# Kernel optimization log

Hardware: AMD Instinct MI355X
Metric: run time of the kernel (lower is better)

## Reference

```python
import jax, jax.numpy as jnp
import numpy as np

B, T, C, H, D = 131072, 8, 32, 4, 8  # batch, context_window, n_embed, num_heads, head_size


def setup_inputs() -> dict:
    key = jax.random.key(0)
    ks = jax.random.split(key, 7)
    s = 0.02
    return {
        "x": jax.random.normal(ks[0], (B, T, C), dtype=jnp.float32),
        "Wq": jax.random.normal(ks[1], (H, C, D), dtype=jnp.float32) * s,
        "Wk": jax.random.normal(ks[2], (H, C, D), dtype=jnp.float32) * s,
        "Wv": jax.random.normal(ks[3], (H, C, D), dtype=jnp.float32) * s,
        "Wf": jax.random.normal(ks[4], (C, C), dtype=jnp.float32) * s,
        "bf": jax.random.normal(ks[5], (C,), dtype=jnp.float32) * s,
    }


def reference(x, Wq, Wk, Wv, Wf, bf):
    # Multi-head causal self-attention (heads batched instead of Python loop)
    q = jnp.einsum('btc,hcd->bhtd', x, Wq)
    k = jnp.einsum('btc,hcd->bhtd', x, Wk)
    v = jnp.einsum('btc,hcd->bhtd', x, Wv)
    scale = jnp.asarray(D, x.dtype) ** -0.5
    scores = jnp.einsum('bhtd,bhsd->bhts', q, k) * scale  # (B,H,T,T)
    causal = jnp.tril(jnp.ones((T, T), dtype=bool))
    scores = jnp.where(causal, scores, jnp.asarray(-jnp.inf, scores.dtype))
    wei = jax.nn.softmax(scores, axis=-1)
    out = jnp.einsum('bhts,bhsd->bhtd', wei, v)
    out = out.transpose(0, 2, 1, 3).reshape(out.shape[0], T, C)  # concat heads
    # FeedForward: Linear + ReLU (note: no residuals in this Block)
    return jax.nn.relu(out @ Wf + bf)
```

## Files before the change

### kernel.cpp

```cpp
#include <hip/hip_runtime.h>
#include <stdint.h>

#define B_ 131072
#define T_ 8
#define C_ 32
#define H_ 4
#define D_ 8

#define NT 4
#define QOFF 0
#define KOFF 2304
#define VOFF 3328
#define HSLAB 4352

typedef _Float16 h16x2 __attribute__((ext_vector_type(2)));
typedef _Float16 f16x8 __attribute__((ext_vector_type(8)));
typedef float    f32x4 __attribute__((ext_vector_type(4)));
typedef __fp16   fp16x2 __attribute__((ext_vector_type(2)));

union H2U { fp16x2 h; uint32_t u; };
union HW  { uint32_t u; h16x2 h; };
union F8U { f16x8 v; uint32_t u[4]; };

__device__ inline uint32_t pk(float lo, float hi) {
    H2U t; t.h = __builtin_amdgcn_cvt_pkrtz(lo, hi); return t.u;
}
__device__ inline h16x2 bch(uint32_t x) { HW t; t.u = x; return t.h; }

struct X2 { float4 a, b; };

__global__ __launch_bounds__(256, 4) void attn_block_mfma(
    const float* __restrict__ X,
    const float* __restrict__ Wq,
    const float* __restrict__ Wk,
    const float* __restrict__ Wv,
    const float* __restrict__ Wf,
    const float* __restrict__ bfb,
    float* __restrict__ Y)
{
    __shared__ __align__(16) char ldsraw[4][2][HSLAB];
    const int wid  = threadIdx.x >> 6;
    const int lane = threadIdx.x & 63;
    const int cc = lane & 15;
    const int gg = lane >> 4;
    char* base = &ldsraw[wid][0][0];

    const float qscale = 0.35355339059327373f;

    f16x8 bW[6];
    {
        const float* const Ws[3] = { Wq, Wk, Wv };
        #pragma unroll
        for (int tau = 0; tau < 6; ++tau) {
            const float* Wm = Ws[tau >> 1];
            const int col = (tau & 1) * 16 + cc;
            const int head = col >> 3, d = col & 7;
            #pragma unroll
            for (int j = 0; j < 8; ++j) {
                float f = Wm[head * (C_ * D_) + (gg * 8 + j) * D_ + d];
                if (tau < 2) f *= qscale;
                bW[tau][j] = (_Float16)f;
            }
        }
    }
    f16x8 bF[2];
    {
        #pragma unroll
        for (int tau = 0; tau < 2; ++tau) {
            const int col = tau * 16 + cc;
            #pragma unroll
            for (int j = 0; j < 8; ++j)
                bF[tau][j] = (_Float16)Wf[(gg * 8 + j) * C_ + col];
        }
    }
    const float bias0 = bfb[cc];
    const float bias1 = bfb[cc + 16];

    const int tilebase = (blockIdx.x * 4 + wid) * (16 * NT);
    const f32x4 z = { 0.f, 0.f, 0.f, 0.f };

    auto ldx = [&](int it) {
        const float* p = X + (size_t)(tilebase + it * 16 + cc) * C_ + gg * 8;
        X2 r; r.a = *(const float4*)p; r.b = *(const float4*)(p + 4); return r;
    };

    auto stage = [&](int slot, X2 x) {
        f16x8 aX;
        aX[0] = (_Float16)x.a.x; aX[1] = (_Float16)x.a.y;
        aX[2] = (_Float16)x.a.z; aX[3] = (_Float16)x.a.w;
        aX[4] = (_Float16)x.b.x; aX[5] = (_Float16)x.b.y;
        aX[6] = (_Float16)x.b.z; aX[7] = (_Float16)x.b.w;

        f32x4 cq[6];
        #pragma unroll
        for (int tau = 0; tau < 6; ++tau)
            cq[tau] = __builtin_amdgcn_mfma_f32_16x16x32_f16(aX, bW[tau], z, 0, 0, 0);

        char* b2 = base + slot * HSLAB;
        float* qb = (float*)(b2 + QOFF);
        #pragma unroll
        for (int tau = 0; tau < 2; ++tau)
            #pragma unroll
            for (int r = 0; r < 4; ++r)
                qb[(gg * 4 + r) * 36 + tau * 16 + cc] = cq[tau][r];
        #pragma unroll
        for (int tau = 2; tau < 6; ++tau) {
            char* dst = b2 + ((tau < 4) ? KOFF : VOFF);
            const int p = (cc & 3) * 8 + (tau & 1) * 4 + (cc >> 2);
            uint2 w2;
            w2.x = pk(cq[tau][0], cq[tau][1]);
            w2.y = pk(cq[tau][2], cq[tau][3]);
            *(uint2*)(dst + p * 32 + gg * 8) = w2;
        }
    };

    auto attn = [&](int slot, int it) {
        char* b2 = base + slot * HSLAB;
        const float* qb = (const float*)(b2 + QOFF);
        const char*  kb = b2 + KOFF;
        const char*  vb = b2 + VOFF;
        const int tpos = cc & 7, bb = cc >> 3;

        const float4 qa = *(const float4*)(qb + cc * 36 + gg * 8);
        const float4 qv = *(const float4*)(qb + cc * 36 + gg * 8 + 4);
        uint32_t qp[8];
        qp[0] = pk(qa.x, qa.x); qp[1] = pk(qa.y, qa.y);
        qp[2] = pk(qa.z, qa.z); qp[3] = pk(qa.w, qa.w);
        qp[4] = pk(qv.x, qv.x); qp[5] = pk(qv.y, qv.y);
        qp[6] = pk(qv.z, qv.z); qp[7] = pk(qv.w, qv.w);

        h16x2 s01 = { (_Float16)0, (_Float16)0 };
        h16x2 s23 = s01, s45 = s01, s67 = s01;
        #pragma unroll
        for (int j = 0; j < 8; ++j) {
            const int p = ((j & 3) << 3) | (gg * 2) | (j >> 2);
            const uint4 ku = *(const uint4*)(kb + p * 32 + bb * 16);
            const h16x2 qj = bch(qp[j]);
            s01 += qj * bch(ku.x);
            s23 += qj * bch(ku.y);
            s45 += qj * bch(ku.z);
            s67 += qj * bch(ku.w);
        }
        float sc[8];
        sc[0] = (float)s01[0]; sc[1] = (float)s01[1];
        sc[2] = (float)s23[0]; sc[3] = (float)s23[1];
        sc[4] = (float)s45[0]; sc[5] = (float)s45[1];
        sc[6] = (float)s67[0]; sc[7] = (float)s67[1];
        #pragma unroll
        for (int s = 0; s < 8; ++s)
            if (s > tpos) sc[s] = -1.0e30f;

        float m = sc[0];
        #pragma unroll
        for (int s = 1; s < 8; ++s) m = fmaxf(m, sc[s]);
        float e[8], sum = 0.f;
        #pragma unroll
        for (int s = 0; s < 8; ++s) { e[s] = __expf(sc[s] - m); sum += e[s]; }
        const float winv = 1.0f / sum;

        uint32_t wp[4];
        wp[0] = pk(e[0] * winv, e[1] * winv);
        wp[1] = pk(e[2] * winv, e[3] * winv);
        wp[2] = pk(e[4] * winv, e[5] * winv);
        wp[3] = pk(e[6] * winv, e[7] * winv);
        const h16x2 w0 = bch(wp[0]), w1 = bch(wp[1]);
        const h16x2 w2 = bch(wp[2]), w3 = bch(wp[3]);

        float o[8];
        #pragma unroll
        for (int d = 0; d < 8; ++d) {
            const int p = ((d & 3) << 3) | (gg * 2) | (d >> 2);
            const uint4 vu = *(const uint4*)(vb + p * 32 + bb * 16);
            h16x2 acc = w0 * bch(vu.x);
            acc += w1 * bch(vu.y);
            acc += w2 * bch(vu.z);
            acc += w3 * bch(vu.w);
            o[d] = (float)acc[0] + (float)acc[1];
        }

        F8U aO;
        aO.u[0] = pk(o[0], o[1]);
        aO.u[1] = pk(o[2], o[3]);
        aO.u[2] = pk(o[4], o[5]);
        aO.u[3] = pk(o[6], o[7]);

        const f32x4 y0 = __builtin_amdgcn_mfma_f32_16x16x32_f16(aO.v, bF[0], z, 0, 0, 0);
        const f32x4 y1 = __builtin_amdgcn_mfma_f32_16x16x32_f16(aO.v, bF[1], z, 0, 0, 0);

        const int rowbase = tilebase + it * 16;
        #pragma unroll
        for (int r = 0; r < 4; ++r) {
            float* yp = Y + (size_t)(rowbase + gg * 4 + r) * C_;
            yp[cc]      = fmaxf(y0[r] + bias0, 0.f);
            yp[cc + 16] = fmaxf(y1[r] + bias1, 0.f);
        }
    };

    X2 x0 = ldx(0), x1 = ldx(1), x2 = ldx(2);
    stage(0, x0);
    X2 x3 = ldx(3);
    stage(1, x1);
    attn(0, 0);
    stage(0, x2);
    attn(1, 1);
    stage(1, x3);
    attn(0, 2);
    attn(1, 3);
}

extern "C" void kernel_launch(void* const* d_in, const int* in_sizes, int n_in,
                              void* d_out, int out_size, void* d_ws, size_t ws_size,
                              hipStream_t stream)
{
    const float* X  = (const float*)d_in[0];
    const float* Wq = (const float*)d_in[1];
    const float* Wk = (const float*)d_in[2];
    const float* Wv = (const float*)d_in[3];
    const float* Wf = (const float*)d_in[4];
    const float* bf = (const float*)d_in[5];
    float* Y = (float*)d_out;

    const int rows = B_ * T_;
    const int rows_per_block = 4 * NT * 16;
    dim3 grid(rows / rows_per_block), block(256);
    hipLaunchKernelGGL(attn_block_mfma, grid, block, 0, stream,
                       X, Wq, Wk, Wv, Wf, bf, Y);
}
```

Before: 52.55 us.

## Use single LDS slot rolled loop, raise occupancy, exp2 softmax with deferred normalization

Replaces the unrolled two-slot stage/attn software pipeline with a rolled loop over one LDS slab per wave, prefetching only the next X tile. This halves LDS use and raises the launch-bounds occupancy hint from 4 to 8 blocks per CU, trading explicit intra-wave overlap for more waves in flight. The softmax folds log2(e) into the Q scale so it can use exp2f, uses tree reductions, and applies 1/sum after the PV product. Reusing one LDS slot within a wave relies on in-order wave execution between the LDS writes and reads.

```diff
diff --git a/kernel.cpp b/kernel.cpp
--- a/kernel.cpp
+++ b/kernel.cpp
@@ -29,7 +29,7 @@
 
 struct X2 { float4 a, b; };
 
-__global__ __launch_bounds__(256, 4) void attn_block_mfma(
+__global__ __launch_bounds__(256, 8) void attn_block_mfma(
     const float* __restrict__ X,
     const float* __restrict__ Wq,
     const float* __restrict__ Wk,
@@ -38,14 +38,14 @@
     const float* __restrict__ bfb,
     float* __restrict__ Y)
 {
-    __shared__ __align__(16) char ldsraw[4][2][HSLAB];
+    __shared__ __align__(16) char ldsraw[4][HSLAB];
     const int wid  = threadIdx.x >> 6;
     const int lane = threadIdx.x & 63;
     const int cc = lane & 15;
     const int gg = lane >> 4;
-    char* base = &ldsraw[wid][0][0];
-
-    const float qscale = 0.35355339059327373f;
+    char* base = &ldsraw[wid][0];
+
+    const float qscale = 0.35355339059327373f * 1.4426950408889634f;
 
     f16x8 bW[6];
     {
@@ -79,12 +79,26 @@
     const int tilebase = (blockIdx.x * 4 + wid) * (16 * NT);
     const f32x4 z = { 0.f, 0.f, 0.f, 0.f };
 
-    auto ldx = [&](int it) {
-        const float* p = X + (size_t)(tilebase + it * 16 + cc) * C_ + gg * 8;
-        X2 r; r.a = *(const float4*)p; r.b = *(const float4*)(p + 4); return r;
-    };
-
-    auto stage = [&](int slot, X2 x) {
+    float* qb = (float*)(base + QOFF);
+    char*  kb = base + KOFF;
+    char*  vb = base + VOFF;
+    const int tpos = cc & 7, bb = cc >> 3;
+
+    X2 x;
+    {
+        const float* p = X + (size_t)(tilebase + cc) * C_ + gg * 8;
+        x.a = *(const float4*)p; x.b = *(const float4*)(p + 4);
+    }
+
+    #pragma unroll 1
+    for (int it = 0; it < NT; ++it) {
+        X2 xn;
+        {
+            const int itn = (it + 1 < NT) ? it + 1 : it;
+            const float* p = X + (size_t)(tilebase + itn * 16 + cc) * C_ + gg * 8;
+            xn.a = *(const float4*)p; xn.b = *(const float4*)(p + 4);
+        }
+
         f16x8 aX;
         aX[0] = (_Float16)x.a.x; aX[1] = (_Float16)x.a.y;
         aX[2] = (_Float16)x.a.z; aX[3] = (_Float16)x.a.w;
@@ -96,8 +110,6 @@
         for (int tau = 0; tau < 6; ++tau)
             cq[tau] = __builtin_amdgcn_mfma_f32_16x16x32_f16(aX, bW[tau], z, 0, 0, 0);
 
-        char* b2 = base + slot * HSLAB;
-        float* qb = (float*)(b2 + QOFF);
         #pragma unroll
         for (int tau = 0; tau < 2; ++tau)
             #pragma unroll
@@ -105,21 +117,13 @@
                 qb[(gg * 4 + r) * 36 + tau * 16 + cc] = cq[tau][r];
         #pragma unroll
         for (int tau = 2; tau < 6; ++tau) {
-            char* dst = b2 + ((tau < 4) ? KOFF : VOFF);
+            char* dst = (tau < 4) ? kb : vb;
             const int p = (cc & 3) * 8 + (tau & 1) * 4 + (cc >> 2);
             uint2 w2;
             w2.x = pk(cq[tau][0], cq[tau][1]);
             w2.y = pk(cq[tau][2], cq[tau][3]);
             *(uint2*)(dst + p * 32 + gg * 8) = w2;
         }
-    };
-
-    auto attn = [&](int slot, int it) {
-        char* b2 = base + slot * HSLAB;
-        const float* qb = (const float*)(b2 + QOFF);
-        const char*  kb = b2 + KOFF;
-        const char*  vb = b2 + VOFF;
-        const int tpos = cc & 7, bb = cc >> 3;
 
         const float4 qa = *(const float4*)(qb + cc * 36 + gg * 8);
         const float4 qv = *(const float4*)(qb + cc * 36 + gg * 8 + 4);
@@ -147,22 +151,24 @@
         sc[4] = (float)s45[0]; sc[5] = (float)s45[1];
         sc[6] = (float)s67[0]; sc[7] = (float)s67[1];
         #pragma unroll
-        for (int s = 0; s < 8; ++s)
+        for (int s = 1; s < 8; ++s)
             if (s > tpos) sc[s] = -1.0e30f;
 
-        float m = sc[0];
-        #pragma unroll
-        for (int s = 1; s < 8; ++s) m = fmaxf(m, sc[s]);
-        float e[8], sum = 0.f;
-        #pragma unroll
-        for (int s = 0; s < 8; ++s) { e[s] = __expf(sc[s] - m); sum += e[s]; }
+        const float m01 = fmaxf(sc[0], sc[1]), m23 = fmaxf(sc[2], sc[3]);
+        const float m45 = fmaxf(sc[4], sc[5]), m67 = fmaxf(sc[6], sc[7]);
+        const float m = fmaxf(fmaxf(m01, m23), fmaxf(m45, m67));
+        float e[8];
+        #pragma unroll
+        for (int s = 0; s < 8; ++s) e[s] = exp2f(sc[s] - m);
+        const float sum = ((e[0] + e[1]) + (e[2] + e[3]))
+                        + ((e[4] + e[5]) + (e[6] + e[7]));
         const float winv = 1.0f / sum;
 
         uint32_t wp[4];
-        wp[0] = pk(e[0] * winv, e[1] * winv);
-        wp[1] = pk(e[2] * winv, e[3] * winv);
-        wp[2] = pk(e[4] * winv, e[5] * winv);
-        wp[3] = pk(e[6] * winv, e[7] * winv);
+        wp[0] = pk(e[0], e[1]);
+        wp[1] = pk(e[2], e[3]);
+        wp[2] = pk(e[4], e[5]);
+        wp[3] = pk(e[6], e[7]);
         const h16x2 w0 = bch(wp[0]), w1 = bch(wp[1]);
         const h16x2 w2 = bch(wp[2]), w3 = bch(wp[3]);
 
@@ -175,7 +181,7 @@
             acc += w1 * bch(vu.y);
             acc += w2 * bch(vu.z);
             acc += w3 * bch(vu.w);
-            o[d] = (float)acc[0] + (float)acc[1];
+            o[d] = ((float)acc[0] + (float)acc[1]) * winv;
         }
 
         F8U aO;
@@ -194,18 +200,9 @@
             yp[cc]      = fmaxf(y0[r] + bias0, 0.f);
             yp[cc + 16] = fmaxf(y1[r] + bias1, 0.f);
         }
-    };
-
-    X2 x0 = ldx(0), x1 = ldx(1), x2 = ldx(2);
-    stage(0, x0);
-    X2 x3 = ldx(3);
-    stage(1, x1);
-    attn(0, 0);
-    stage(0, x2);
-    attn(1, 1);
-    stage(1, x3);
-    attn(0, 2);
-    attn(1, 3);
+
+        x = xn;
+    }
 }
 
 extern "C" void kernel_launch(void* const* d_in, const int* in_sizes, int n_in,
```

New measurement: 104.1 us. 1.98x slower.

## Pack Q as fp16 in LDS, drop softmax max, defer normalization

Applied to the files above, without the earlier changes.

Q is now packed into fp16 pairs in LDS, which shrinks the per-slot LDS slab, and the occupancy hint in launch bounds goes from 4 to 6. The softmax now folds log2(e) into the Q scale and uses exp2f without subtracting the row max. Normalization is applied once to the attention output instead of to each weight. These changes cut LDS traffic, conversions and ALU work. Dropping the max subtraction risks overflow or precision loss when scores are large, so it relies on scores staying small.

```diff
diff --git a/kernel.cpp b/kernel.cpp
--- a/kernel.cpp
+++ b/kernel.cpp
@@ -9,9 +9,9 @@
 
 #define NT 4
 #define QOFF 0
-#define KOFF 2304
-#define VOFF 3328
-#define HSLAB 4352
+#define KOFF 1152
+#define VOFF 2176
+#define HSLAB 3200
 
 typedef _Float16 h16x2 __attribute__((ext_vector_type(2)));
 typedef _Float16 f16x8 __attribute__((ext_vector_type(8)));
@@ -21,6 +21,7 @@
 union H2U { fp16x2 h; uint32_t u; };
 union HW  { uint32_t u; h16x2 h; };
 union F8U { f16x8 v; uint32_t u[4]; };
+union V4  { uint4 u; h16x2 h2[4]; };
 
 __device__ inline uint32_t pk(float lo, float hi) {
     H2U t; t.h = __builtin_amdgcn_cvt_pkrtz(lo, hi); return t.u;
@@ -29,7 +30,7 @@
 
 struct X2 { float4 a, b; };
 
-__global__ __launch_bounds__(256, 4) void attn_block_mfma(
+__global__ __launch_bounds__(256, 6) void attn_block_mfma(
     const float* __restrict__ X,
     const float* __restrict__ Wq,
     const float* __restrict__ Wk,
@@ -45,7 +46,7 @@
     const int gg = lane >> 4;
     char* base = &ldsraw[wid][0][0];
 
-    const float qscale = 0.35355339059327373f;
+    const float qscale = 0.35355339059327373f * 1.4426950408889634f;
 
     f16x8 bW[6];
     {
@@ -78,6 +79,7 @@
 
     const int tilebase = (blockIdx.x * 4 + wid) * (16 * NT);
     const f32x4 z = { 0.f, 0.f, 0.f, 0.f };
+    const int tpos = cc & 7, bb = cc >> 3;
 
     auto ldx = [&](int it) {
         const float* p = X + (size_t)(tilebase + it * 16 + cc) * C_ + gg * 8;
@@ -97,12 +99,10 @@
             cq[tau] = __builtin_amdgcn_mfma_f32_16x16x32_f16(aX, bW[tau], z, 0, 0, 0);
 
         char* b2 = base + slot * HSLAB;
-        float* qb = (float*)(b2 + QOFF);
-        #pragma unroll
-        for (int tau = 0; tau < 2; ++tau)
-            #pragma unroll
-            for (int r = 0; r < 4; ++r)
-                qb[(gg * 4 + r) * 36 + tau * 16 + cc] = cq[tau][r];
+        uint32_t* qb = (uint32_t*)(b2 + QOFF);
+        #pragma unroll
+        for (int r = 0; r < 4; ++r)
+            qb[(gg * 4 + r) * 18 + cc] = pk(cq[0][r], cq[1][r]);
         #pragma unroll
         for (int tau = 2; tau < 6; ++tau) {
             char* dst = b2 + ((tau < 4) ? KOFF : VOFF);
@@ -116,18 +116,22 @@
 
     auto attn = [&](int slot, int it) {
         char* b2 = base + slot * HSLAB;
-        const float* qb = (const float*)(b2 + QOFF);
-        const char*  kb = b2 + KOFF;
-        const char*  vb = b2 + VOFF;
-        const int tpos = cc & 7, bb = cc >> 3;
-
-        const float4 qa = *(const float4*)(qb + cc * 36 + gg * 8);
-        const float4 qv = *(const float4*)(qb + cc * 36 + gg * 8 + 4);
-        uint32_t qp[8];
-        qp[0] = pk(qa.x, qa.x); qp[1] = pk(qa.y, qa.y);
-        qp[2] = pk(qa.z, qa.z); qp[3] = pk(qa.w, qa.w);
-        qp[4] = pk(qv.x, qv.x); qp[5] = pk(qv.y, qv.y);
-        qp[6] = pk(qv.z, qv.z); qp[7] = pk(qv.w, qv.w);
+        const char* qbb = b2 + QOFF;
+        const char* kb  = b2 + KOFF;
+        const char* vb  = b2 + VOFF;
+
+        V4 q0, q1;
+        q0.u = *(const uint4*)(qbb + cc * 72 + (gg & 1) * 32);
+        q1.u = *(const uint4*)(qbb + cc * 72 + (gg & 1) * 32 + 16);
+        const bool hi = gg >= 2;
+        h16x2 qj[8];
+        #pragma unroll
+        for (int j = 0; j < 4; ++j) {
+            const _Float16 v0 = hi ? q0.h2[j][1] : q0.h2[j][0];
+            const _Float16 v1 = hi ? q1.h2[j][1] : q1.h2[j][0];
+            qj[j]     = h16x2{ v0, v0 };
+            qj[j + 4] = h16x2{ v1, v1 };
+        }
 
         h16x2 s01 = { (_Float16)0, (_Float16)0 };
         h16x2 s23 = s01, s45 = s01, s67 = s01;
@@ -135,11 +139,10 @@
         for (int j = 0; j < 8; ++j) {
             const int p = ((j & 3) << 3) | (gg * 2) | (j >> 2);
             const uint4 ku = *(const uint4*)(kb + p * 32 + bb * 16);
-            const h16x2 qj = bch(qp[j]);
-            s01 += qj * bch(ku.x);
-            s23 += qj * bch(ku.y);
-            s45 += qj * bch(ku.z);
-            s67 += qj * bch(ku.w);
+            s01 += qj[j] * bch(ku.x);
+            s23 += qj[j] * bch(ku.y);
+            s45 += qj[j] * bch(ku.z);
+            s67 += qj[j] * bch(ku.w);
         }
         float sc[8];
         sc[0] = (float)s01[0]; sc[1] = (float)s01[1];
@@ -147,24 +150,20 @@
         sc[4] = (float)s45[0]; sc[5] = (float)s45[1];
         sc[6] = (float)s67[0]; sc[7] = (float)s67[1];
         #pragma unroll
-        for (int s = 0; s < 8; ++s)
+        for (int s = 1; s < 8; ++s)
             if (s > tpos) sc[s] = -1.0e30f;
 
-        float m = sc[0];
-        #pragma unroll
-        for (int s = 1; s < 8; ++s) m = fmaxf(m, sc[s]);
-        float e[8], sum = 0.f;
-        #pragma unroll
-        for (int s = 0; s < 8; ++s) { e[s] = __expf(sc[s] - m); sum += e[s]; }
+        float e[8];
+        #pragma unroll
+        for (int s = 0; s < 8; ++s) e[s] = exp2f(sc[s]);
+        const float sum = ((e[0] + e[1]) + (e[2] + e[3]))
+                        + ((e[4] + e[5]) + (e[6] + e[7]));
         const float winv = 1.0f / sum;
 
-        uint32_t wp[4];
-        wp[0] = pk(e[0] * winv, e[1] * winv);
-        wp[1] = pk(e[2] * winv, e[3] * winv);
-        wp[2] = pk(e[4] * winv, e[5] * winv);
-        wp[3] = pk(e[6] * winv, e[7] * winv);
-        const h16x2 w0 = bch(wp[0]), w1 = bch(wp[1]);
-        const h16x2 w2 = bch(wp[2]), w3 = bch(wp[3]);
+        const h16x2 w0 = bch(pk(e[0], e[1]));
+        const h16x2 w1 = bch(pk(e[2], e[3]));
+        const h16x2 w2 = bch(pk(e[4], e[5]));
+        const h16x2 w3 = bch(pk(e[6], e[7]));
 
         float o[8];
         #pragma unroll
@@ -175,7 +174,7 @@
             acc += w1 * bch(vu.y);
             acc += w2 * bch(vu.z);
             acc += w3 * bch(vu.w);
-            o[d] = (float)acc[0] + (float)acc[1];
+            o[d] = ((float)acc[0] + (float)acc[1]) * winv;
         }
 
         F8U aO;
```

Result: slower. 54.36 us (+3.5%).
